# Performance work log

Hardware: AMD Instinct MI355X
Metric: run time of the kernel (lower is better)

Reference implementation:

```python
import jax, jax.numpy as jnp
import numpy as np


def setup_inputs() -> dict:
    key = jax.random.key(0)
    ks = jax.random.split(key, 6)
    B, T, H, U = 32, 2048, 1024, 1024
    return {
        "query": jax.random.normal(ks[0], (1, B, H), dtype=jnp.float32),
        "values": jax.random.normal(ks[1], (B, T, H), dtype=jnp.float32),
        "W_w": jax.random.normal(ks[2], (U, 2 * H), dtype=jnp.float32) * (1.0 / np.sqrt(2 * H)),
        "W_b": jax.random.normal(ks[3], (U,), dtype=jnp.float32) * 0.02,
        "V_w": jax.random.normal(ks[4], (1, U), dtype=jnp.float32) * (1.0 / np.sqrt(U)),
        "V_b": jax.random.normal(ks[5], (1,), dtype=jnp.float32) * 0.02,
    }


def reference(query, values, W_w, W_b, V_w, V_b):
    # query: [1, B, H] -> [B, H]; values: [B, T, H]
    q = query[0]  # squeeze dim 0
    H = values.shape[-1]
    # Split W over the concat dim instead of materializing cat([values, q_rep]):
    # cat @ W.T == values @ W[:, :H].T + q @ W[:, H:].T  (same math as torch)
    Wv, Wq = W_w[:, :H], W_w[:, H:]
    pre = (jnp.einsum("bth,uh->btu", values, Wv)
           + jnp.einsum("bh,uh->bu", q, Wq)[:, None, :]
           + W_b)  # [B, T, U]
    score = jnp.tanh(pre) @ V_w[0] + V_b[0]  # [B, T]
    attention_weights = jax.nn.softmax(score, axis=1)[..., None]  # [B, T, 1]
    context_vector = jnp.sum(attention_weights * values, axis=1)  # [B, H]
    return (context_vector, attention_weights)
```

## Files before the change

kernel.cpp:

```cpp
#include <hip/hip_runtime.h>
#include <hip/hip_bf16.h>


#define B_DIM 32
#define T_DIM 2048
#define H_DIM 1024
#define U_DIM 1024

typedef __bf16 bf16x8 __attribute__((ext_vector_type(8)));
typedef float f32x4 __attribute__((ext_vector_type(4)));

__device__ __forceinline__ unsigned short f2bf(float f) {
    unsigned int u = __float_as_uint(f);
    unsigned int r = (u + 0x7FFFu + ((u >> 16) & 1u)) >> 16;
    return (unsigned short)r;
}

__global__ void prep_wv_kernel(const float* __restrict__ W_w,
                               unsigned short* __restrict__ wv) {
    int u = blockIdx.x;
    int tid = threadIdx.x;
    float4 x = reinterpret_cast<const float4*>(W_w + (size_t)u * 2 * H_DIM)[tid];
    uint2 p;
    p.x = (unsigned int)f2bf(x.x) | ((unsigned int)f2bf(x.y) << 16);
    p.y = (unsigned int)f2bf(x.z) | ((unsigned int)f2bf(x.w) << 16);
    reinterpret_cast<uint2*>(wv)[(size_t)u * (H_DIM / 4) + tid] = p;
}

__global__ void prep_c_kernel(const float* __restrict__ q,
                              const float* __restrict__ W_w,
                              const float* __restrict__ W_b,
                              float* __restrict__ cvec) {
    __shared__ float q_sh[H_DIM];
    int b = blockIdx.y;
    int u0 = blockIdx.x * 128;
    int tid = threadIdx.x;
    for (int i = tid; i < H_DIM / 4; i += 128)
        reinterpret_cast<float4*>(q_sh)[i] =
            reinterpret_cast<const float4*>(q + (size_t)b * H_DIM)[i];
    __syncthreads();
    int u = u0 + tid;
    const float4* wrow = reinterpret_cast<const float4*>(W_w + (size_t)u * 2 * H_DIM + H_DIM);
    float s = 0.f;
#pragma unroll 4
    for (int i = 0; i < H_DIM / 4; i++) {
        float4 wv4 = wrow[i];
        float4 q4 = reinterpret_cast<float4*>(q_sh)[i];
        s += wv4.x * q4.x + wv4.y * q4.y + wv4.z * q4.z + wv4.w * q4.w;
    }
    cvec[(size_t)b * U_DIM + u] = s + W_b[u];
}

__global__ __launch_bounds__(512, 2)
void gemm_score_kernel(const float* __restrict__ values,
                       const unsigned short* __restrict__ wv,
                       const float* __restrict__ cvec,
                       const float* __restrict__ Vw,
                       float* __restrict__ score) {
    __shared__ unsigned short a_sh[64 * 40];
    __shared__ float sc_sh[64 * 8];

    const int tid = threadIdx.x;
    const int lane = tid & 63;
    const int w = tid >> 6;
    const int col = lane & 15;
    const int quad = lane >> 4;
    const int m0 = blockIdx.x * 64;
    const int b = m0 >> 11;
    const int t0 = m0 & (T_DIM - 1);

    f32x4 acc[4][8];
    const f32x4 zero4 = {0.f, 0.f, 0.f, 0.f};
#pragma unroll
    for (int mt = 0; mt < 4; mt++)
#pragma unroll
        for (int nt = 0; nt < 8; nt++) acc[mt][nt] = zero4;

    const int srow = tid >> 3;
    const int scol = (tid & 7) * 4;
    const float* arow = values + (size_t)(m0 + srow) * H_DIM + scol;
    const unsigned short* bbase = wv + (size_t)(w * 128 + col) * H_DIM + quad * 8;

    float4 v = *reinterpret_cast<const float4*>(arow);
    bf16x8 bnext[8];
#pragma unroll
    for (int nt = 0; nt < 8; nt++)
        bnext[nt] = *reinterpret_cast<const bf16x8*>(bbase + (size_t)nt * 16 * H_DIM);

    for (int k0 = 0; k0 < H_DIM; k0 += 32) {
        __syncthreads();
        uint2 p;
        p.x = (unsigned int)f2bf(v.x) | ((unsigned int)f2bf(v.y) << 16);
        p.y = (unsigned int)f2bf(v.z) | ((unsigned int)f2bf(v.w) << 16);
        *reinterpret_cast<uint2*>(&a_sh[srow * 40 + scol]) = p;
        __syncthreads();

        bf16x8 bcur[8];
#pragma unroll
        for (int nt = 0; nt < 8; nt++) bcur[nt] = bnext[nt];

        const int k1 = (k0 + 32) & (H_DIM - 1);
        v = *reinterpret_cast<const float4*>(arow + k1);
#pragma unroll
        for (int nt = 0; nt < 8; nt++)
            bnext[nt] = *reinterpret_cast<const bf16x8*>(bbase + (size_t)nt * 16 * H_DIM + k1);

        bf16x8 af[4];
#pragma unroll
        for (int mt = 0; mt < 4; mt++)
            af[mt] = *reinterpret_cast<const bf16x8*>(&a_sh[(mt * 16 + col) * 40 + quad * 8]);

#pragma unroll
        for (int nt = 0; nt < 8; nt++)
#pragma unroll
            for (int mt = 0; mt < 4; mt++)
                acc[mt][nt] = __builtin_amdgcn_mfma_f32_16x16x32_bf16(af[mt], bcur[nt],
                                                                      acc[mt][nt], 0, 0, 0);
    }

    float cv[8], vwv[8];
#pragma unroll
    for (int nt = 0; nt < 8; nt++) {
        int n = w * 128 + nt * 16 + col;
        cv[nt] = cvec[(size_t)b * U_DIM + n];
        vwv[nt] = Vw[n];
    }
#pragma unroll
    for (int mt = 0; mt < 4; mt++) {
#pragma unroll
        for (int j = 0; j < 4; j++) {
            float s = 0.f;
#pragma unroll
            for (int nt = 0; nt < 8; nt++)
                s += tanhf(acc[mt][nt][j] + cv[nt]) * vwv[nt];
            s += __shfl_xor(s, 1, 64);
            s += __shfl_xor(s, 2, 64);
            s += __shfl_xor(s, 4, 64);
            s += __shfl_xor(s, 8, 64);
            if (col == 0) sc_sh[(mt * 16 + quad * 4 + j) * 8 + w] = s;
        }
    }
    __syncthreads();
    if (tid < 64) {
        float s = 0.f;
#pragma unroll
        for (int ww = 0; ww < 8; ww++) s += sc_sh[tid * 8 + ww];
        score[(size_t)b * T_DIM + t0 + tid] = s;
    }
}

__global__ void softmax_kernel(const float* __restrict__ score,
                               float* __restrict__ aw) {
    int b = blockIdx.x;
    int tid = threadIdx.x;
    int lane = tid & 63, w = tid >> 6;
    __shared__ float redm[4];
    __shared__ float reds[4];
    float loc[8];
    float m = -1e30f;
#pragma unroll
    for (int i = 0; i < 8; i++) {
        loc[i] = score[(size_t)b * T_DIM + tid + i * 256];
        m = fmaxf(m, loc[i]);
    }
#pragma unroll
    for (int off = 32; off >= 1; off >>= 1) m = fmaxf(m, __shfl_xor(m, off, 64));
    if (lane == 0) redm[w] = m;
    __syncthreads();
    m = fmaxf(fmaxf(redm[0], redm[1]), fmaxf(redm[2], redm[3]));
    float sum = 0.f;
#pragma unroll
    for (int i = 0; i < 8; i++) {
        loc[i] = __expf(loc[i] - m);
        sum += loc[i];
    }
#pragma unroll
    for (int off = 32; off >= 1; off >>= 1) sum += __shfl_xor(sum, off, 64);
    if (lane == 0) reds[w] = sum;
    __syncthreads();
    sum = reds[0] + reds[1] + reds[2] + reds[3];
    float inv = 1.0f / sum;
#pragma unroll
    for (int i = 0; i < 8; i++)
        aw[(size_t)b * T_DIM + tid + i * 256] = loc[i] * inv;
}

__global__ void ctx_partial_kernel(const float* __restrict__ values,
                                   const float* __restrict__ aw,
                                   float* __restrict__ partial) {
    int tc = blockIdx.x;
    int b = blockIdx.y;
    int tid = threadIdx.x;
    const float4* v4 = reinterpret_cast<const float4*>(
                           values + ((size_t)b * T_DIM + tc * 128) * H_DIM) + tid;
    const float* a = aw + (size_t)b * T_DIM + tc * 128;
    float4 acc = make_float4(0.f, 0.f, 0.f, 0.f);
#pragma unroll 4
    for (int t = 0; t < 128; t++) {
        float wgt = a[t];
        float4 vv = v4[(size_t)t * (H_DIM / 4)];
        acc.x += wgt * vv.x; acc.y += wgt * vv.y;
        acc.z += wgt * vv.z; acc.w += wgt * vv.w;
    }
    reinterpret_cast<float4*>(partial + ((size_t)b * 16 + tc) * H_DIM)[tid] = acc;
}

__global__ void ctx_combine_kernel(const float* __restrict__ partial,
                                   float* __restrict__ ctx) {
    int idx = blockIdx.x * 256 + threadIdx.x;
    int b = idx >> 10, h = idx & (H_DIM - 1);
    float s = 0.f;
#pragma unroll
    for (int tc = 0; tc < 16; tc++)
        s += partial[((size_t)b * 16 + tc) * H_DIM + h];
    ctx[idx] = s;
}

extern "C" void kernel_launch(void* const* d_in, const int* in_sizes, int n_in,
                              void* d_out, int out_size, void* d_ws, size_t ws_size,
                              hipStream_t stream) {
    const float* query  = (const float*)d_in[0];
    const float* values = (const float*)d_in[1];
    const float* W_w    = (const float*)d_in[2];
    const float* W_b    = (const float*)d_in[3];
    const float* V_w    = (const float*)d_in[4];

    float* out = (float*)d_out;
    char* ws = (char*)d_ws;
    float* cvec            = (float*)(ws);
    unsigned short* wv     = (unsigned short*)(ws + 131072);
    float* score           = (float*)(ws + 131072 + 2097152);
    float* partial         = (float*)(ws + 131072 + 2097152 + 262144);
    float* ctx = out;
    float* aw  = out + B_DIM * H_DIM;

    prep_wv_kernel<<<U_DIM, 256, 0, stream>>>(W_w, wv);
    prep_c_kernel<<<dim3(8, B_DIM), 128, 0, stream>>>(query, W_w, (const float*)d_in[3], cvec);
    gemm_score_kernel<<<(B_DIM * T_DIM) / 64, 512, 0, stream>>>(values, wv, cvec, V_w, score);
    softmax_kernel<<<B_DIM, 256, 0, stream>>>(score, aw);
    ctx_partial_kernel<<<dim3(16, B_DIM), 256, 0, stream>>>(values, aw, partial);
    ctx_combine_kernel<<<128, 256, 0, stream>>>(partial, ctx);
}
```

Measured before the change: 712.8 us.

## Double-buffer A tile with 64-wide K steps, fast tanh, warp-per-row query projection

The GEMM main loop now uses a double-buffered LDS tile covering 64 K elements per step, with one barrier per step instead of two. The next values chunk is prefetched before the MFMAs and stored into the other buffer afterward. tanhf is replaced with an exp/reciprocal approximation, and the query projection kernel is restructured so each wavefront reduces whole W rows with coalesced loads and shuffles. Risks include higher register pressure from the 16 B fragments held per step and a small accuracy change from the approximate tanh.

```diff
diff --git a/kernel.cpp b/kernel.cpp
--- a/kernel.cpp
+++ b/kernel.cpp
@@ -10,10 +10,15 @@
 typedef __bf16 bf16x8 __attribute__((ext_vector_type(8)));
 typedef float f32x4 __attribute__((ext_vector_type(4)));
 
-__device__ __forceinline__ unsigned short f2bf(float f) {
+__device__ __forceinline__ unsigned int f2bf(float f) {
     unsigned int u = __float_as_uint(f);
-    unsigned int r = (u + 0x7FFFu + ((u >> 16) & 1u)) >> 16;
-    return (unsigned short)r;
+    return (u + 0x7FFFu + ((u >> 16) & 1u)) >> 16;
+}
+
+__device__ __forceinline__ float fast_tanh(float x) {
+    x = fminf(9.f, fmaxf(-9.f, x));
+    float e = __expf(2.f * x);
+    return 1.f - 2.f * __frcp_rn(e + 1.f);
 }
 
 __global__ void prep_wv_kernel(const float* __restrict__ W_w,
@@ -22,8 +27,8 @@
     int tid = threadIdx.x;
     float4 x = reinterpret_cast<const float4*>(W_w + (size_t)u * 2 * H_DIM)[tid];
     uint2 p;
-    p.x = (unsigned int)f2bf(x.x) | ((unsigned int)f2bf(x.y) << 16);
-    p.y = (unsigned int)f2bf(x.z) | ((unsigned int)f2bf(x.w) << 16);
+    p.x = f2bf(x.x) | (f2bf(x.y) << 16);
+    p.y = f2bf(x.z) | (f2bf(x.w) << 16);
     reinterpret_cast<uint2*>(wv)[(size_t)u * (H_DIM / 4) + tid] = p;
 }
 
@@ -31,24 +36,28 @@
                               const float* __restrict__ W_w,
                               const float* __restrict__ W_b,
                               float* __restrict__ cvec) {
-    __shared__ float q_sh[H_DIM];
+    __shared__ float4 q_sh[H_DIM / 4];
     int b = blockIdx.y;
-    int u0 = blockIdx.x * 128;
-    int tid = threadIdx.x;
-    for (int i = tid; i < H_DIM / 4; i += 128)
-        reinterpret_cast<float4*>(q_sh)[i] =
-            reinterpret_cast<const float4*>(q + (size_t)b * H_DIM)[i];
-    __syncthreads();
-    int u = u0 + tid;
-    const float4* wrow = reinterpret_cast<const float4*>(W_w + (size_t)u * 2 * H_DIM + H_DIM);
-    float s = 0.f;
-#pragma unroll 4
-    for (int i = 0; i < H_DIM / 4; i++) {
-        float4 wv4 = wrow[i];
-        float4 q4 = reinterpret_cast<float4*>(q_sh)[i];
-        s += wv4.x * q4.x + wv4.y * q4.y + wv4.z * q4.z + wv4.w * q4.w;
-    }
-    cvec[(size_t)b * U_DIM + u] = s + W_b[u];
+    int u0 = blockIdx.x * 64;
+    int tid = threadIdx.x;
+    int lane = tid & 63, w = tid >> 6;
+    q_sh[tid] = reinterpret_cast<const float4*>(q + (size_t)b * H_DIM)[tid];
+    __syncthreads();
+#pragma unroll
+    for (int i = 0; i < 16; i++) {
+        int u = u0 + w * 16 + i;
+        const float4* wr = reinterpret_cast<const float4*>(W_w + (size_t)u * 2 * H_DIM + H_DIM);
+        float s = 0.f;
+#pragma unroll
+        for (int j = 0; j < 4; j++) {
+            float4 wv4 = wr[j * 64 + lane];
+            float4 q4 = q_sh[j * 64 + lane];
+            s += wv4.x * q4.x + wv4.y * q4.y + wv4.z * q4.z + wv4.w * q4.w;
+        }
+#pragma unroll
+        for (int off = 32; off >= 1; off >>= 1) s += __shfl_xor(s, off, 64);
+        if (lane == 0) cvec[(size_t)b * U_DIM + u] = s + W_b[u];
+    }
 }
 
 __global__ __launch_bounds__(512, 2)
@@ -57,7 +66,7 @@
                        const float* __restrict__ cvec,
                        const float* __restrict__ Vw,
                        float* __restrict__ score) {
-    __shared__ unsigned short a_sh[64 * 40];
+    __shared__ __align__(16) unsigned short a_sh[2][64 * 72];
     __shared__ float sc_sh[64 * 8];
 
     const int tid = threadIdx.x;
@@ -77,45 +86,66 @@
         for (int nt = 0; nt < 8; nt++) acc[mt][nt] = zero4;
 
     const int srow = tid >> 3;
-    const int scol = (tid & 7) * 4;
-    const float* arow = values + (size_t)(m0 + srow) * H_DIM + scol;
+    const int skg = tid & 7;
+    const float* aptr = values + (size_t)(m0 + srow) * H_DIM + skg * 8;
+    const int sidx = srow * 72 + skg * 8;
+
+    {
+        float4 n0 = reinterpret_cast<const float4*>(aptr)[0];
+        float4 n1 = reinterpret_cast<const float4*>(aptr)[1];
+        uint4 pk;
+        pk.x = f2bf(n0.x) | (f2bf(n0.y) << 16);
+        pk.y = f2bf(n0.z) | (f2bf(n0.w) << 16);
+        pk.z = f2bf(n1.x) | (f2bf(n1.y) << 16);
+        pk.w = f2bf(n1.z) | (f2bf(n1.w) << 16);
+        *reinterpret_cast<uint4*>(&a_sh[0][sidx]) = pk;
+    }
+    __syncthreads();
+
     const unsigned short* bbase = wv + (size_t)(w * 128 + col) * H_DIM + quad * 8;
 
-    float4 v = *reinterpret_cast<const float4*>(arow);
-    bf16x8 bnext[8];
-#pragma unroll
-    for (int nt = 0; nt < 8; nt++)
-        bnext[nt] = *reinterpret_cast<const bf16x8*>(bbase + (size_t)nt * 16 * H_DIM);
-
-    for (int k0 = 0; k0 < H_DIM; k0 += 32) {
+    for (int ks = 0; ks < 16; ks++) {
+        const int cur = ks & 1;
+
+        float4 n0, n1;
+        if (ks < 15) {
+            const float* ap = aptr + (ks + 1) * 64;
+            n0 = reinterpret_cast<const float4*>(ap)[0];
+            n1 = reinterpret_cast<const float4*>(ap)[1];
+        }
+
+        bf16x8 bf[2][8];
+#pragma unroll
+        for (int kk = 0; kk < 2; kk++)
+#pragma unroll
+            for (int nt = 0; nt < 8; nt++)
+                bf[kk][nt] = *reinterpret_cast<const bf16x8*>(
+                    bbase + (size_t)nt * 16 * H_DIM + ks * 64 + kk * 32);
+
+#pragma unroll
+        for (int kk = 0; kk < 2; kk++) {
+            bf16x8 af[4];
+#pragma unroll
+            for (int mt = 0; mt < 4; mt++)
+                af[mt] = *reinterpret_cast<const bf16x8*>(
+                    &a_sh[cur][(mt * 16 + col) * 72 + kk * 32 + quad * 8]);
+#pragma unroll
+            for (int nt = 0; nt < 8; nt++)
+#pragma unroll
+                for (int mt = 0; mt < 4; mt++)
+                    acc[mt][nt] = __builtin_amdgcn_mfma_f32_16x16x32_bf16(
+                        af[mt], bf[kk][nt], acc[mt][nt], 0, 0, 0);
+        }
+
+        if (ks < 15) {
+            uint4 pk;
+            pk.x = f2bf(n0.x) | (f2bf(n0.y) << 16);
+            pk.y = f2bf(n0.z) | (f2bf(n0.w) << 16);
+            pk.z = f2bf(n1.x) | (f2bf(n1.y) << 16);
+            pk.w = f2bf(n1.z) | (f2bf(n1.w) << 16);
+            *reinterpret_cast<uint4*>(&a_sh[1 - cur][sidx]) = pk;
+        }
         __syncthreads();
-        uint2 p;
-        p.x = (unsigned int)f2bf(v.x) | ((unsigned int)f2bf(v.y) << 16);
-        p.y = (unsigned int)f2bf(v.z) | ((unsigned int)f2bf(v.w) << 16);
-        *reinterpret_cast<uint2*>(&a_sh[srow * 40 + scol]) = p;
-        __syncthreads();
-
-        bf16x8 bcur[8];
-#pragma unroll
-        for (int nt = 0; nt < 8; nt++) bcur[nt] = bnext[nt];
-
-        const int k1 = (k0 + 32) & (H_DIM - 1);
-        v = *reinterpret_cast<const float4*>(arow + k1);
-#pragma unroll
-        for (int nt = 0; nt < 8; nt++)
-            bnext[nt] = *reinterpret_cast<const bf16x8*>(bbase + (size_t)nt * 16 * H_DIM + k1);
-
-        bf16x8 af[4];
-#pragma unroll
-        for (int mt = 0; mt < 4; mt++)
-            af[mt] = *reinterpret_cast<const bf16x8*>(&a_sh[(mt * 16 + col) * 40 + quad * 8]);
-
-#pragma unroll
-        for (int nt = 0; nt < 8; nt++)
-#pragma unroll
-            for (int mt = 0; mt < 4; mt++)
-                acc[mt][nt] = __builtin_amdgcn_mfma_f32_16x16x32_bf16(af[mt], bcur[nt],
-                                                                      acc[mt][nt], 0, 0, 0);
     }
 
     float cv[8], vwv[8];
@@ -132,7 +162,7 @@
             float s = 0.f;
 #pragma unroll
             for (int nt = 0; nt < 8; nt++)
-                s += tanhf(acc[mt][nt][j] + cv[nt]) * vwv[nt];
+                s += fast_tanh(acc[mt][nt][j] + cv[nt]) * vwv[nt];
             s += __shfl_xor(s, 1, 64);
             s += __shfl_xor(s, 2, 64);
             s += __shfl_xor(s, 4, 64);
@@ -235,7 +265,7 @@
     float* aw  = out + B_DIM * H_DIM;
 
     prep_wv_kernel<<<U_DIM, 256, 0, stream>>>(W_w, wv);
-    prep_c_kernel<<<dim3(8, B_DIM), 128, 0, stream>>>(query, W_w, (const float*)d_in[3], cvec);
+    prep_c_kernel<<<dim3(U_DIM / 64, B_DIM), 256, 0, stream>>>(query, W_w, W_b, cvec);
     gemm_score_kernel<<<(B_DIM * T_DIM) / 64, 512, 0, stream>>>(values, wv, cvec, V_w, score);
     softmax_kernel<<<B_DIM, 256, 0, stream>>>(score, aw);
     ctx_partial_kernel<<<dim3(16, B_DIM), 256, 0, stream>>>(values, aw, partial);
```

New measurement: 675.0 us. 1.06x faster.
